# Kernel tuning notes

Measured on AMD Instinct MI355X. Metric: run time of the kernel, lower is better.

Reference implementation:

```python
import jax, jax.numpy as jnp
import numpy as np

D = 128        # d_model
VOCAB = 2000   # vocab_size
NUM_ITERS = 6
NUM_V = 98304  # total vertices = 3 * num_edges
NUM_E = NUM_V // 3


def setup_inputs() -> dict:
    key = jax.random.key(0)
    ks = jax.random.split(key, 20)
    std = 0.02
    inp = {
        "x_v": jax.random.randint(ks[0], (NUM_V,), 0, VOCAB),
        "target_mask": jax.random.randint(ks[1], (NUM_V,), 0, 2) > 0,
        # embedding table (vocab_size + 1 rows, last is padding idx)
        "emb": jax.random.normal(ks[2], (VOCAB + 1, D), jnp.float32) * std,
        # edge_init: Linear(1, d_model)
        "edge_init_w": jax.random.normal(ks[3], (D, 1), jnp.float32) * std,
        "edge_init_b": jnp.zeros((D,), jnp.float32),
        # vertex_to_edge LSTM(3d -> d): torch gate order i,f,g,o
        "Wih_v2e": jax.random.normal(ks[4], (4 * D, 3 * D), jnp.float32) * (1.0 / np.sqrt(D)),
        "Whh_v2e": jax.random.normal(ks[5], (4 * D, D), jnp.float32) * (1.0 / np.sqrt(D)),
        "bih_v2e": jax.random.normal(ks[6], (4 * D,), jnp.float32) * (1.0 / np.sqrt(D)),
        "bhh_v2e": jax.random.normal(ks[7], (4 * D,), jnp.float32) * (1.0 / np.sqrt(D)),
        # edge_to_vertex: 3 position-specific LSTM(d -> d), stacked along axis 0
        "Wih_e2v": jax.random.normal(ks[8], (3, 4 * D, D), jnp.float32) * (1.0 / np.sqrt(D)),
        "Whh_e2v": jax.random.normal(ks[9], (3, 4 * D, D), jnp.float32) * (1.0 / np.sqrt(D)),
        "bih_e2v": jax.random.normal(ks[10], (3, 4 * D), jnp.float32) * (1.0 / np.sqrt(D)),
        "bhh_e2v": jax.random.normal(ks[11], (3, 4 * D), jnp.float32) * (1.0 / np.sqrt(D)),
        # output projection Linear(d -> vocab)
        "out_w": jax.random.normal(ks[12], (VOCAB, D), jnp.float32) * std,
        "out_b": jnp.zeros((VOCAB,), jnp.float32),
    }
    return inp


def _lstm_cell(gates, c):
    # torch LSTM gate order: input, forget, cell(g), output
    i, f, g, o = jnp.split(gates, 4, axis=-1)
    c_new = jax.nn.sigmoid(f) * c + jax.nn.sigmoid(i) * jnp.tanh(g)
    h_new = jax.nn.sigmoid(o) * jnp.tanh(c_new)
    return h_new, c_new


def reference(x_v, target_mask, emb, edge_init_w, edge_init_b,
              Wih_v2e, Whh_v2e, bih_v2e, bhh_v2e,
              Wih_e2v, Whh_e2v, bih_e2v, bhh_e2v,
              out_w, out_b):
    E = x_v.shape[0] // 3
    # init embeddings (-1 ids would map to padding row VOCAB; ids are in-range here)
    h_v = emb[x_v].reshape(E, 3, D)              # [E, 3, D]
    c_v = jnp.zeros_like(h_v)
    h_e = jnp.broadcast_to(edge_init_w[:, 0] + edge_init_b, (E, D))  # Linear(1->D) on ones
    c_e = jnp.zeros_like(h_e)
    mask = target_mask.reshape(E, 3)[..., None]  # [E, 3, 1]
    b_v2e = bih_v2e + bhh_v2e                    # [4D]
    b_e2v = (bih_e2v + bhh_e2v)[None]            # [1, 3, 4D]

    for _ in range(NUM_ITERS):
        # vertex -> edge: concat 3 vertices, one LSTM cell step
        msg = h_v.reshape(E, 3 * D)
        gates_e = msg @ Wih_v2e.T + h_e @ Whh_v2e.T + b_v2e          # [E, 4D]
        h_e, c_e = _lstm_cell(gates_e, c_e)
        # edge -> vertex: 3 position-specific LSTM cells, same edge input
        gates_v = (jnp.einsum('ed,pkd->epk', h_e, Wih_e2v)
                   + jnp.einsum('epd,pkd->epk', h_v, Whh_e2v)
                   + b_e2v)                                          # [E, 3, 4D]
        h_new, c_new = _lstm_cell(gates_v, c_v)
        h_v = jnp.where(mask, h_new, h_v)
        c_v = jnp.where(mask, c_new, c_v)

    logits = h_v.reshape(3 * E, D) @ out_w.T + out_b                 # [3E, VOCAB]
    return logits
```

## Files before the change

kernel.cpp:

```cpp
#include <hip/hip_runtime.h>

#define E_CNT 32768
#define V_CNT 98304
#define D_ 128
#define VOCAB_ 2000
#define ITERS_ 6

typedef unsigned short u16;
typedef _Float16 f16;
typedef __attribute__((ext_vector_type(8))) _Float16 f16x8;
typedef __attribute__((ext_vector_type(4))) float f32x4;

__device__ __forceinline__ f32x4 MFh(f16x8 a, f16x8 b, f32x4 c) {
    return __builtin_amdgcn_mfma_f32_16x16x32_f16(a, b, c, 0, 0, 0);
}
__device__ __forceinline__ float sigmoid_f(float x) {
    return __builtin_amdgcn_rcpf(1.0f + __expf(-x));
}
__device__ __forceinline__ float tanh_f(float x) {
    float ax = fabsf(x);
    float t = fmaf(-2.0f, __builtin_amdgcn_rcpf(__expf(2.0f * ax) + 1.0f), 1.0f);
    return copysignf(t, x);
}

__global__ void detect_mask_kernel(const unsigned int* __restrict__ m, int* __restrict__ flag) {
    int i = blockIdx.x * 256 + threadIdx.x;
    if (i < 4096 && m[i] > 1u) atomicOr(flag, 1);
}

__global__ void prep_kernel(
    const float* __restrict__ Wih_v2e, const float* __restrict__ Whh_v2e,
    const float* __restrict__ bih_v2e, const float* __restrict__ bhh_v2e,
    const float* __restrict__ Wih_e2v, const float* __restrict__ Whh_e2v,
    const float* __restrict__ bih_e2v, const float* __restrict__ bhh_e2v,
    const float* __restrict__ out_w,
    f16* __restrict__ WvF, f16* __restrict__ WeF,
    f16* __restrict__ OwFh, f16* __restrict__ OwFl,
    float* __restrict__ bv, float* __restrict__ be)
{
    int idx = blockIdx.x * 256 + threadIdx.x;
    if (idx < 262144) {
        const int r = idx & 7, l = (idx >> 3) & 63, t = idx >> 9;
        const int kk = t & 15, nt = t >> 4;
        const int j = nt * 16 + (l & 15);
        const int k = kk * 32 + (l >> 4) * 8 + r;
        const float w = (k < 384) ? Wih_v2e[j * 384 + k] : Whh_v2e[j * 128 + (k - 384)];
        WvF[idx] = (f16)w;
        return;
    }
    idx -= 262144;
    if (idx < 393216) {
        const int r = idx & 7, l = (idx >> 3) & 63, t = idx >> 9;
        const int kk = t & 7, nt = (t >> 3) & 31, p = t >> 8;
        const int j = nt * 16 + (l & 15);
        const int k = kk * 32 + (l >> 4) * 8 + r;
        const float w = (k < 128) ? Wih_e2v[(p * 512 + j) * 128 + k]
                                  : Whh_e2v[(p * 512 + j) * 128 + (k - 128)];
        WeF[idx] = (f16)w;
        return;
    }
    idx -= 393216;
    if (idx < 256000) {
        const int r = idx & 7, l = (idx >> 3) & 63, t = idx >> 9;
        const int kk = t & 3, nt = t >> 2;
        const int j = nt * 16 + (l & 15);
        const int k = kk * 32 + (l >> 4) * 8 + r;
        const float w = out_w[j * 128 + k];
        const f16 h = (f16)w;
        OwFh[idx] = h;
        OwFl[idx] = (f16)(w - (float)h);
        return;
    }
    idx -= 256000;
    if (idx < 512) { bv[idx] = bih_v2e[idx] + bhh_v2e[idx]; return; }
    idx -= 512;
    if (idx < 1536) { be[idx] = bih_e2v[idx] + bhh_e2v[idx]; return; }
}

__global__ __launch_bounds__(512)
void fused_kernel(
    const int* __restrict__ x_v,
    const float* __restrict__ emb,
    const float* __restrict__ eiw, const float* __restrict__ eib,
    const f16* __restrict__ WvF, const f16* __restrict__ WeF,
    const float* __restrict__ bv, const float* __restrict__ be,
    const void* __restrict__ mask, const int* __restrict__ flagp,
    float* __restrict__ cvG,
    f16* __restrict__ hvOut)
{
    __shared__ f16 HV[24576];
    __shared__ f16 HE[8192];

    const int tid = threadIdx.x;
    const int c = tid >> 6, l = tid & 63;
    const int lr = l & 15, lk = l >> 4;
    const int e0 = blockIdx.x * 64;

    for (int i = tid; i < 64 * 48; i += 512) {
        const int row = i / 48, seg = i % 48;
        int id = x_v[(e0 + row) * 3 + (seg >> 4)];
        if (id < 0 || id > VOCAB_) id = VOCAB_;
        const float* s = emb + id * D_ + ((seg * 8) & 127);
        float4 a = *(const float4*)s, b = *(const float4*)(s + 4);
        f16x8 H;
        H[0] = (f16)a.x; H[1] = (f16)a.y; H[2] = (f16)a.z; H[3] = (f16)a.w;
        H[4] = (f16)b.x; H[5] = (f16)b.y; H[6] = (f16)b.z; H[7] = (f16)b.w;
        *(f16x8*)&HV[((row >> 4) * 12 + (seg >> 2)) * 512 + (seg & 3) * 128 + (row & 15) * 8] = H;
    }
    for (int i = tid; i < 64 * 16; i += 512) {
        const int row = i / 16, seg = i % 16;
        f16x8 H;
        #pragma unroll
        for (int j = 0; j < 8; ++j) H[j] = (f16)(eiw[seg * 8 + j] + eib[seg * 8 + j]);
        *(f16x8*)&HE[((row >> 4) * 4 + (seg >> 2)) * 512 + (seg & 3) * 128 + (row & 15) * 8] = H;
    }

    const int isByte = *flagp;
    unsigned mbits[3];
    #pragma unroll
    for (int p = 0; p < 3; ++p) {
        unsigned mb = 0;
        #pragma unroll
        for (int mt = 0; mt < 4; ++mt)
            #pragma unroll
            for (int r = 0; r < 4; ++r) {
                const int v = (e0 + mt * 16 + lk * 4 + r) * 3 + p;
                const bool m = isByte ? (((const unsigned char*)mask)[v] != 0)
                                      : (((const int*)mask)[v] != 0);
                mb |= (unsigned)m << (mt * 4 + r);
            }
        mbits[p] = mb;
    }
    const int d = c * 16 + lr;
    const int wBase = (c >> 1) * 512 + ((c & 1) * 2 + (lr >> 3)) * 128 + lk * 32 + (lr & 7);
    float ce[4][4];
    #pragma unroll
    for (int mt = 0; mt < 4; ++mt)
        #pragma unroll
        for (int r = 0; r < 4; ++r) ce[mt][r] = 0.0f;

    __syncthreads();

    const f16* HVl = HV + l * 8;
    const f16* HEl = HE + l * 8;

    #pragma unroll 1
    for (int it = 0; it < ITERS_; ++it) {
        {
            f32x4 acc[4][4];
            #pragma unroll
            for (int mt = 0; mt < 4; ++mt)
                #pragma unroll
                for (int g = 0; g < 4; ++g) acc[mt][g] = (f32x4)0.0f;

            f16x8 Bc[4];
            #pragma unroll
            for (int g = 0; g < 4; ++g)
                Bc[g] = *(const f16x8*)(WvF + (((g * 8 + c) * 16) * 64 + l) * 8);

            #pragma unroll 2
            for (int kk = 0; kk < 16; ++kk) {
                f16x8 Bn[4];
                if (kk < 15) {
                    #pragma unroll
                    for (int g = 0; g < 4; ++g)
                        Bn[g] = *(const f16x8*)(WvF + (((g * 8 + c) * 16 + kk + 1) * 64 + l) * 8);
                }
                f16x8 Ah[4];
                if (kk < 12) {
                    #pragma unroll
                    for (int mt = 0; mt < 4; ++mt)
                        Ah[mt] = *(const f16x8*)(HVl + (mt * 12 + kk) * 512);
                } else {
                    #pragma unroll
                    for (int mt = 0; mt < 4; ++mt)
                        Ah[mt] = *(const f16x8*)(HEl + (mt * 4 + (kk - 12)) * 512);
                }
                #pragma unroll
                for (int g = 0; g < 4; ++g)
                    #pragma unroll
                    for (int mt = 0; mt < 4; ++mt)
                        acc[mt][g] = MFh(Ah[mt], Bc[g], acc[mt][g]);
                #pragma unroll
                for (int g = 0; g < 4; ++g) Bc[g] = Bn[g];
            }
            __syncthreads();
            const float bvi = bv[d], bvf = bv[128 + d], bvg = bv[256 + d], bvo = bv[384 + d];
            #pragma unroll
            for (int mt = 0; mt < 4; ++mt)
                #pragma unroll
                for (int r = 0; r < 4; ++r) {
                    float gi = sigmoid_f(acc[mt][0][r] + bvi);
                    float gf = sigmoid_f(acc[mt][1][r] + bvf);
                    float gg = tanh_f(acc[mt][2][r] + bvg);
                    float go = sigmoid_f(acc[mt][3][r] + bvo);
                    float cn = gf * ce[mt][r] + gi * gg;
                    ce[mt][r] = cn;
                    HE[wBase + mt * 2048 + r * 8] = (f16)(go * tanh_f(cn));
                }
            __syncthreads();
        }
        #pragma unroll 1
        for (int p = 0; p < 3; ++p) {
            f32x4 acc[4][4];
            #pragma unroll
            for (int mt = 0; mt < 4; ++mt)
                #pragma unroll
                for (int g = 0; g < 4; ++g) acc[mt][g] = (f32x4)0.0f;

            f16x8 Bc[4];
            #pragma unroll
            for (int g = 0; g < 4; ++g)
                Bc[g] = *(const f16x8*)(WeF + ((((p * 32) + (g * 8 + c)) * 8) * 64 + l) * 8);

            #pragma unroll 2
            for (int kk = 0; kk < 8; ++kk) {
                f16x8 Bn[4];
                if (kk < 7) {
                    #pragma unroll
                    for (int g = 0; g < 4; ++g)
                        Bn[g] = *(const f16x8*)(WeF + ((((p * 32) + (g * 8 + c)) * 8 + kk + 1) * 64 + l) * 8);
                }
                f16x8 Ah[4];
                if (kk < 4) {
                    #pragma unroll
                    for (int mt = 0; mt < 4; ++mt)
                        Ah[mt] = *(const f16x8*)(HEl + (mt * 4 + kk) * 512);
                } else {
                    #pragma unroll
                    for (int mt = 0; mt < 4; ++mt)
                        Ah[mt] = *(const f16x8*)(HVl + (mt * 12 + 4 * p + (kk - 4)) * 512);
                }
                #pragma unroll
                for (int g = 0; g < 4; ++g)
                    #pragma unroll
                    for (int mt = 0; mt < 4; ++mt)
                        acc[mt][g] = MFh(Ah[mt], Bc[g], acc[mt][g]);
                #pragma unroll
                for (int g = 0; g < 4; ++g) Bc[g] = Bn[g];
            }
            __syncthreads();
            const float bei = be[p * 512 + d], bef = be[p * 512 + 128 + d];
            const float beg = be[p * 512 + 256 + d], beo = be[p * 512 + 384 + d];
            #pragma unroll
            for (int mt = 0; mt < 4; ++mt)
                #pragma unroll
                for (int r = 0; r < 4; ++r) {
                    if ((mbits[p] >> (mt * 4 + r)) & 1u) {
                        float gi = sigmoid_f(acc[mt][0][r] + bei);
                        float gf = sigmoid_f(acc[mt][1][r] + bef);
                        float gg = tanh_f(acc[mt][2][r] + beg);
                        float go = sigmoid_f(acc[mt][3][r] + beo);
                        const int row = mt * 16 + lk * 4 + r;
                        const size_t co = ((size_t)(e0 + row) * 3 + p) * 128 + d;
                        float cvold = (it == 0) ? 0.0f : cvG[co];
                        float cn = gf * cvold + gi * gg;
                        cvG[co] = cn;
                        HV[wBase + mt * 6144 + p * 2048 + r * 8] = (f16)(go * tanh_f(cn));
                    }
                }
        }
        __syncthreads();
    }

    for (int i = tid; i < 64 * 48; i += 512) {
        const int row = i / 48, seg = i % 48;
        *(f16x8*)&hvOut[(size_t)(e0 + row) * 384 + seg * 8] =
            *(const f16x8*)&HV[((row >> 4) * 12 + (seg >> 2)) * 512 + (seg & 3) * 128 + (row & 15) * 8];
    }
}

__global__ __launch_bounds__(512) void proj_kernel(
    const f16* __restrict__ hv,
    const f16* __restrict__ WFh, const f16* __restrict__ WFl,
    const float* __restrict__ out_b, float* __restrict__ out)
{
    __shared__ char occ_pad[81920];
    const int tid = threadIdx.x, l = tid & 63;
    occ_pad[tid] = (char)tid;
    __syncthreads();
    {
        int keep = (int)occ_pad[(tid + 1) & 511];
        asm volatile("" :: "v"(keep));
    }

    const int wid = blockIdx.x * 8 + (tid >> 6);
    const int v0 = wid * 32;
    const int lr = l & 15, lk = l >> 4;

    f16x8 Bv[2][4];
    #pragma unroll
    for (int vt = 0; vt < 2; ++vt)
        #pragma unroll
        for (int kk = 0; kk < 4; ++kk)
            Bv[vt][kk] = *(const f16x8*)(hv + (v0 + vt * 16 + lr) * D_ + kk * 32 + lk * 8);

    f16x8 Wc[8];
    #pragma unroll
    for (int kk = 0; kk < 4; ++kk) {
        Wc[kk]     = *(const f16x8*)(WFh + ((kk) * 64 + l) * 8);
        Wc[4 + kk] = *(const f16x8*)(WFl + ((kk) * 64 + l) * 8);
    }

    #pragma unroll 2
    for (int nt = 0; nt < 125; ++nt) {
        f16x8 Wn[8];
        if (nt < 124) {
            #pragma unroll
            for (int kk = 0; kk < 4; ++kk) {
                const int fb = (((nt + 1) * 4 + kk) * 64 + l) * 8;
                Wn[kk]     = *(const f16x8*)(WFh + fb);
                Wn[4 + kk] = *(const f16x8*)(WFl + fb);
            }
        }
        f32x4 t0 = (f32x4)0.0f, t1 = (f32x4)0.0f, u0 = (f32x4)0.0f, u1 = (f32x4)0.0f;
        #pragma unroll
        for (int kk = 0; kk < 4; ++kk) {
            t0 = MFh(Wc[kk], Bv[0][kk], t0);
            t1 = MFh(Wc[kk], Bv[1][kk], t1);
            u0 = MFh(Wc[4 + kk], Bv[0][kk], u0);
            u1 = MFh(Wc[4 + kk], Bv[1][kk], u1);
        }
        f32x4 a0 = t0 + u0;
        f32x4 a1 = t1 + u1;
        const int n0 = nt * 16 + lk * 4;
        const float4 bb = *(const float4*)&out_b[n0];
        {
            const size_t v = (size_t)(v0 + lr);
            float4 o = make_float4(a0[0] + bb.x, a0[1] + bb.y, a0[2] + bb.z, a0[3] + bb.w);
            *(float4*)&out[v * VOCAB_ + n0] = o;
        }
        {
            const size_t v = (size_t)(v0 + 16 + lr);
            float4 o = make_float4(a1[0] + bb.x, a1[1] + bb.y, a1[2] + bb.z, a1[3] + bb.w);
            *(float4*)&out[v * VOCAB_ + n0] = o;
        }
        #pragma unroll
        for (int q = 0; q < 8; ++q) Wc[q] = Wn[q];
    }
}

extern "C" void kernel_launch(void* const* d_in, const int* in_sizes, int n_in,
                              void* d_out, int out_size, void* d_ws, size_t ws_size,
                              hipStream_t stream)
{
    const int*   x_v     = (const int*)  d_in[0];
    const void*  mask    = d_in[1];
    const float* emb     = (const float*)d_in[2];
    const float* eiw     = (const float*)d_in[3];
    const float* eib     = (const float*)d_in[4];
    const float* Wih_v2e = (const float*)d_in[5];
    const float* Whh_v2e = (const float*)d_in[6];
    const float* bih_v2e = (const float*)d_in[7];
    const float* bhh_v2e = (const float*)d_in[8];
    const float* Wih_e2v = (const float*)d_in[9];
    const float* Whh_e2v = (const float*)d_in[10];
    const float* bih_e2v = (const float*)d_in[11];
    const float* bhh_e2v = (const float*)d_in[12];
    const float* out_w   = (const float*)d_in[13];
    const float* out_b   = (const float*)d_in[14];
    float* out = (float*)d_out;

    char* ws = (char*)d_ws;
    f16*   hv   = (f16*)(ws);
    f16*   WvF  = (f16*)(ws + 25165824);
    f16*   WeF  = (f16*)(ws + 25690112);
    f16*   OwFh = (f16*)(ws + 26476544);
    f16*   OwFl = (f16*)(ws + 26988544);
    float* bv   = (float*)(ws + 27500544);
    float* be   = (float*)(ws + 27502592);
    int*   flag = (int*)(ws + 27508736);
    float* cvG  = (float*)(ws + 27525120);

    hipMemsetAsync(flag, 0, 4, stream);
    detect_mask_kernel<<<16, 256, 0, stream>>>((const unsigned int*)mask, flag);
    prep_kernel<<<3568, 256, 0, stream>>>(Wih_v2e, Whh_v2e, bih_v2e, bhh_v2e,
                                          Wih_e2v, Whh_e2v, bih_e2v, bhh_e2v, out_w,
                                          WvF, WeF, OwFh, OwFl, bv, be);
    fused_kernel<<<E_CNT / 64, 512, 0, stream>>>(x_v, emb, eiw, eib,
                                                 WvF, WeF, bv, be,
                                                 mask, flag, cvG, hv);
    proj_kernel<<<V_CNT / 256, 512, 0, stream>>>(hv, OwFh, OwFl, out_b, out);
}
```

Before: 786.7 us.

## Drop split-fp16 output weights, coalesce cell-state storage, simplify weight loads

New measurement: 794.0 us. No clear change (+0.9%).

```diff
diff --git a/kernel.cpp b/kernel.cpp
--- a/kernel.cpp
+++ b/kernel.cpp
@@ -34,8 +34,7 @@
     const float* __restrict__ Wih_e2v, const float* __restrict__ Whh_e2v,
     const float* __restrict__ bih_e2v, const float* __restrict__ bhh_e2v,
     const float* __restrict__ out_w,
-    f16* __restrict__ WvF, f16* __restrict__ WeF,
-    f16* __restrict__ OwFh, f16* __restrict__ OwFl,
+    f16* __restrict__ WvF, f16* __restrict__ WeF, f16* __restrict__ OwF,
     float* __restrict__ bv, float* __restrict__ be)
 {
     int idx = blockIdx.x * 256 + threadIdx.x;
@@ -65,10 +64,7 @@
         const int kk = t & 3, nt = t >> 2;
         const int j = nt * 16 + (l & 15);
         const int k = kk * 32 + (l >> 4) * 8 + r;
-        const float w = out_w[j * 128 + k];
-        const f16 h = (f16)w;
-        OwFh[idx] = h;
-        OwFl[idx] = (f16)(w - (float)h);
+        OwF[idx] = (f16)out_w[j * 128 + k];
         return;
     }
     idx -= 256000;
@@ -85,7 +81,7 @@
     const f16* __restrict__ WvF, const f16* __restrict__ WeF,
     const float* __restrict__ bv, const float* __restrict__ be,
     const void* __restrict__ mask, const int* __restrict__ flagp,
-    float* __restrict__ cvG,
+    float4* __restrict__ cvG4,
     f16* __restrict__ hvOut)
 {
     __shared__ f16 HV[24576];
@@ -143,6 +139,7 @@
 
     const f16* HVl = HV + l * 8;
     const f16* HEl = HE + l * 8;
+    const size_t cvBase = (size_t)blockIdx.x * 12 * 512 + tid;
 
     #pragma unroll 1
     for (int it = 0; it < ITERS_; ++it) {
@@ -153,19 +150,8 @@
                 #pragma unroll
                 for (int g = 0; g < 4; ++g) acc[mt][g] = (f32x4)0.0f;
 
-            f16x8 Bc[4];
-            #pragma unroll
-            for (int g = 0; g < 4; ++g)
-                Bc[g] = *(const f16x8*)(WvF + (((g * 8 + c) * 16) * 64 + l) * 8);
-
             #pragma unroll 2
             for (int kk = 0; kk < 16; ++kk) {
-                f16x8 Bn[4];
-                if (kk < 15) {
-                    #pragma unroll
-                    for (int g = 0; g < 4; ++g)
-                        Bn[g] = *(const f16x8*)(WvF + (((g * 8 + c) * 16 + kk + 1) * 64 + l) * 8);
-                }
                 f16x8 Ah[4];
                 if (kk < 12) {
                     #pragma unroll
@@ -177,12 +163,12 @@
                         Ah[mt] = *(const f16x8*)(HEl + (mt * 4 + (kk - 12)) * 512);
                 }
                 #pragma unroll
-                for (int g = 0; g < 4; ++g)
-                    #pragma unroll
-                    for (int mt = 0; mt < 4; ++mt)
-                        acc[mt][g] = MFh(Ah[mt], Bc[g], acc[mt][g]);
-                #pragma unroll
-                for (int g = 0; g < 4; ++g) Bc[g] = Bn[g];
+                for (int g = 0; g < 4; ++g) {
+                    f16x8 B = *(const f16x8*)(WvF + (((g * 8 + c) * 16 + kk) * 64 + l) * 8);
+                    #pragma unroll
+                    for (int mt = 0; mt < 4; ++mt)
+                        acc[mt][g] = MFh(Ah[mt], B, acc[mt][g]);
+                }
             }
             __syncthreads();
             const float bvi = bv[d], bvf = bv[128 + d], bvg = bv[256 + d], bvo = bv[384 + d];
@@ -208,19 +194,8 @@
                 #pragma unroll
                 for (int g = 0; g < 4; ++g) acc[mt][g] = (f32x4)0.0f;
 
-            f16x8 Bc[4];
-            #pragma unroll
-            for (int g = 0; g < 4; ++g)
-                Bc[g] = *(const f16x8*)(WeF + ((((p * 32) + (g * 8 + c)) * 8) * 64 + l) * 8);
-
             #pragma unroll 2
             for (int kk = 0; kk < 8; ++kk) {
-                f16x8 Bn[4];
-                if (kk < 7) {
-                    #pragma unroll
-                    for (int g = 0; g < 4; ++g)
-                        Bn[g] = *(const f16x8*)(WeF + ((((p * 32) + (g * 8 + c)) * 8 + kk + 1) * 64 + l) * 8);
-                }
                 f16x8 Ah[4];
                 if (kk < 4) {
                     #pragma unroll
@@ -229,21 +204,27 @@
                 } else {
                     #pragma unroll
                     for (int mt = 0; mt < 4; ++mt)
-                        Ah[mt] = *(const f16x8*)(HVl + (mt * 12 + 4 * p + (kk - 4)) * 512);
-                }
-                #pragma unroll
-                for (int g = 0; g < 4; ++g)
-                    #pragma unroll
-                    for (int mt = 0; mt < 4; ++mt)
-                        acc[mt][g] = MFh(Ah[mt], Bc[g], acc[mt][g]);
-                #pragma unroll
-                for (int g = 0; g < 4; ++g) Bc[g] = Bn[g];
+                        Ah[mt] = *(const f16x8*)(HVl + (mt * 12 + p * 4 + (kk - 4)) * 512);
+                }
+                #pragma unroll
+                for (int g = 0; g < 4; ++g) {
+                    f16x8 B = *(const f16x8*)(WeF + ((((p * 32) + (g * 8 + c)) * 8 + kk) * 64 + l) * 8);
+                    #pragma unroll
+                    for (int mt = 0; mt < 4; ++mt)
+                        acc[mt][g] = MFh(Ah[mt], B, acc[mt][g]);
+                }
             }
             __syncthreads();
             const float bei = be[p * 512 + d], bef = be[p * 512 + 128 + d];
             const float beg = be[p * 512 + 256 + d], beo = be[p * 512 + 384 + d];
             #pragma unroll
-            for (int mt = 0; mt < 4; ++mt)
+            for (int mt = 0; mt < 4; ++mt) {
+                const size_t ci = cvBase + (p * 4 + mt) * 512;
+                float cvv[4] = {0.0f, 0.0f, 0.0f, 0.0f};
+                if (it > 0) {
+                    float4 t = cvG4[ci];
+                    cvv[0] = t.x; cvv[1] = t.y; cvv[2] = t.z; cvv[3] = t.w;
+                }
                 #pragma unroll
                 for (int r = 0; r < 4; ++r) {
                     if ((mbits[p] >> (mt * 4 + r)) & 1u) {
@@ -251,14 +232,13 @@
                         float gf = sigmoid_f(acc[mt][1][r] + bef);
                         float gg = tanh_f(acc[mt][2][r] + beg);
                         float go = sigmoid_f(acc[mt][3][r] + beo);
-                        const int row = mt * 16 + lk * 4 + r;
-                        const size_t co = ((size_t)(e0 + row) * 3 + p) * 128 + d;
-                        float cvold = (it == 0) ? 0.0f : cvG[co];
-                        float cn = gf * cvold + gi * gg;
-                        cvG[co] = cn;
+                        float cn = gf * cvv[r] + gi * gg;
+                        cvv[r] = cn;
                         HV[wBase + mt * 6144 + p * 2048 + r * 8] = (f16)(go * tanh_f(cn));
                     }
                 }
+                cvG4[ci] = make_float4(cvv[0], cvv[1], cvv[2], cvv[3]);
+            }
         }
         __syncthreads();
     }
@@ -270,21 +250,20 @@
     }
 }
 
-__global__ __launch_bounds__(512) void proj_kernel(
-    const f16* __restrict__ hv,
-    const f16* __restrict__ WFh, const f16* __restrict__ WFl,
+__global__ __launch_bounds__(256) void proj_kernel(
+    const f16* __restrict__ hv, const f16* __restrict__ WF,
     const float* __restrict__ out_b, float* __restrict__ out)
 {
-    __shared__ char occ_pad[81920];
+    __shared__ char occ_pad[49152];
     const int tid = threadIdx.x, l = tid & 63;
     occ_pad[tid] = (char)tid;
     __syncthreads();
     {
-        int keep = (int)occ_pad[(tid + 1) & 511];
+        int keep = (int)occ_pad[(tid + 1) & 255];
         asm volatile("" :: "v"(keep));
     }
 
-    const int wid = blockIdx.x * 8 + (tid >> 6);
+    const int wid = blockIdx.x * 4 + (tid >> 6);
     const int v0 = wid * 32;
     const int lr = l & 15, lk = l >> 4;
 
@@ -295,34 +274,25 @@
         for (int kk = 0; kk < 4; ++kk)
             Bv[vt][kk] = *(const f16x8*)(hv + (v0 + vt * 16 + lr) * D_ + kk * 32 + lk * 8);
 
-    f16x8 Wc[8];
+    f16x8 Wc[4];
     #pragma unroll
-    for (int kk = 0; kk < 4; ++kk) {
-        Wc[kk]     = *(const f16x8*)(WFh + ((kk) * 64 + l) * 8);
-        Wc[4 + kk] = *(const f16x8*)(WFl + ((kk) * 64 + l) * 8);
-    }
+    for (int kk = 0; kk < 4; ++kk)
+        Wc[kk] = *(const f16x8*)(WF + (kk * 64 + l) * 8);
 
     #pragma unroll 2
     for (int nt = 0; nt < 125; ++nt) {
-        f16x8 Wn[8];
+        f16x8 Wn[4];
         if (nt < 124) {
             #pragma unroll
-            for (int kk = 0; kk < 4; ++kk) {
-                const int fb = (((nt + 1) * 4 + kk) * 64 + l) * 8;
-                Wn[kk]     = *(const f16x8*)(WFh + fb);
-                Wn[4 + kk] = *(const f16x8*)(WFl + fb);
-            }
-        }
-        f32x4 t0 = (f32x4)0.0f, t1 = (f32x4)0.0f, u0 = (f32x4)0.0f, u1 = (f32x4)0.0f;
+            for (int kk = 0; kk < 4; ++kk)
+                Wn[kk] = *(const f16x8*)(WF + (((nt + 1) * 4 + kk) * 64 + l) * 8);
+        }
+        f32x4 a0 = (f32x4)0.0f, a1 = (f32x4)0.0f;
         #pragma unroll
         for (int kk = 0; kk < 4; ++kk) {
-            t0 = MFh(Wc[kk], Bv[0][kk], t0);
-            t1 = MFh(Wc[kk], Bv[1][kk], t1);
-            u0 = MFh(Wc[4 + kk], Bv[0][kk], u0);
-            u1 = MFh(Wc[4 + kk], Bv[1][kk], u1);
-        }
-        f32x4 a0 = t0 + u0;
-        f32x4 a1 = t1 + u1;
+            a0 = MFh(Wc[kk], Bv[0][kk], a0);
+            a1 = MFh(Wc[kk], Bv[1][kk], a1);
+        }
         const int n0 = nt * 16 + lk * 4;
         const float4 bb = *(const float4*)&out_b[n0];
         {
@@ -336,7 +306,7 @@
             *(float4*)&out[v * VOCAB_ + n0] = o;
         }
         #pragma unroll
-        for (int q = 0; q < 8; ++q) Wc[q] = Wn[q];
+        for (int q = 0; q < 4; ++q) Wc[q] = Wn[q];
     }
 }
 
@@ -362,23 +332,22 @@
     float* out = (float*)d_out;
 
     char* ws = (char*)d_ws;
-    f16*   hv   = (f16*)(ws);
-    f16*   WvF  = (f16*)(ws + 25165824);
-    f16*   WeF  = (f16*)(ws + 25690112);
-    f16*   OwFh = (f16*)(ws + 26476544);
-    f16*   OwFl = (f16*)(ws + 26988544);
-    float* bv   = (float*)(ws + 27500544);
-    float* be   = (float*)(ws + 27502592);
-    int*   flag = (int*)(ws + 27508736);
-    float* cvG  = (float*)(ws + 27525120);
+    f16*    hv   = (f16*)(ws);
+    f16*    WvF  = (f16*)(ws + 25165824);
+    f16*    WeF  = (f16*)(ws + 25690112);
+    f16*    OwF  = (f16*)(ws + 26476544);
+    float*  bv   = (float*)(ws + 26988544);
+    float*  be   = (float*)(ws + 26990592);
+    int*    flag = (int*)(ws + 26996736);
+    float4* cvG4 = (float4*)(ws + 27000832);
 
     hipMemsetAsync(flag, 0, 4, stream);
     detect_mask_kernel<<<16, 256, 0, stream>>>((const unsigned int*)mask, flag);
     prep_kernel<<<3568, 256, 0, stream>>>(Wih_v2e, Whh_v2e, bih_v2e, bhh_v2e,
                                           Wih_e2v, Whh_e2v, bih_e2v, bhh_e2v, out_w,
-                                          WvF, WeF, OwFh, OwFl, bv, be);
+                                          WvF, WeF, OwF, bv, be);
     fused_kernel<<<E_CNT / 64, 512, 0, stream>>>(x_v, emb, eiw, eib,
                                                  WvF, WeF, bv, be,
-                                                 mask, flag, cvG, hv);
-    proj_kernel<<<V_CNT / 256, 512, 0, stream>>>(hv, OwFh, OwFl, out_b, out);
-}
+                                                 mask, flag, cvG4, hv);
+    proj_kernel<<<V_CNT / 128, 256, 0, stream>>>(hv, OwF, out_b, out);
+}
```
